# Optimization experiments

Measured on AMD Instinct MI355X. Metric: run time of the kernel, lower is better.

The kernel has to match this reference:

```python
import jax, jax.numpy as jnp
import numpy as np

MAX_NUM_ATOMS = 128  # static stand-in for tf's data-dependent max(pair_indices)+1


def setup_inputs() -> dict:
    key = jax.random.key(0)
    k1, k2 = jax.random.split(key)
    B, M, F = 32, 4096, 64
    edge_features = jax.random.normal(k1, (B, M, F), dtype=jnp.float32)
    pair_indices = jax.random.randint(k2, (B, M, 2), 0, MAX_NUM_ATOMS).astype(jnp.int64)
    return {"edge_features": edge_features, "pair_indices": pair_indices}


def reference(edge_features, pair_indices):
    # edge_features: [B, M, F]; pair_indices: [B, M, 2] with values in [0, N)
    B, M, F = edge_features.shape
    N = MAX_NUM_ATOMS
    b_idx = jnp.broadcast_to(jnp.arange(B)[:, None], (B, M))  # batch index per edge
    i_idx = pair_indices[..., 0]
    j_idx = pair_indices[..., 1]
    out = jnp.zeros((B, N, N, F), dtype=edge_features.dtype)
    # scatter-add each edge feature into dense [B, N, N, F] adjacency-feature tensor
    out = out.at[b_idx, i_idx, j_idx].add(edge_features)
    return out
```

## Files before the change

### kernel.cpp

```cpp
#include <hip/hip_runtime.h>

constexpr int B_DIM   = 32;
constexpr int M_EDGES = 4096;
constexpr int F_DIM   = 64;
constexpr int N_ATOMS = 128;

constexpr int TOTAL_EDGES = B_DIM * M_EDGES;
constexpr int CELLS       = B_DIM * N_ATOMS * N_ATOMS;
constexpr int K_CAP       = 16;

__global__ __launch_bounds__(256) void bin_edges_kernel(
    const int* __restrict__ pair,
    int*       __restrict__ counts,
    unsigned int* __restrict__ list)
{
    const int e = blockIdx.x * 256 + threadIdx.x;
    if (e >= TOTAL_EDGES) return;

    const int2 ij = ((const int2*)pair)[e];
    const int b = e >> 12;

    const int cell = (b << 14) + (ij.x << 7) + ij.y;

    const int pos = atomicAdd(&counts[cell], 1);
    if (pos < K_CAP) list[cell * K_CAP + pos] = (unsigned int)e;
}

__global__ __launch_bounds__(256) void gather_write_kernel(
    const float*        __restrict__ edge,
    const int*          __restrict__ counts,
    const unsigned int* __restrict__ list,
    float*              __restrict__ out)
{
    const int tid  = blockIdx.x * 256 + threadIdx.x;
    const int cell = tid >> 4;
    const int q    = tid & 15;

    int cnt = counts[cell];
    cnt = cnt > K_CAP ? K_CAP : cnt;

    float4 acc = make_float4(0.f, 0.f, 0.f, 0.f);
    const unsigned int* cl = list + (size_t)cell * K_CAP;

    for (int t = 0; t < cnt; ++t) {
        const unsigned int e = cl[t];
        const float4 v = ((const float4*)edge)[(size_t)e * 16 + q];
        acc.x += v.x; acc.y += v.y; acc.z += v.z; acc.w += v.w;
    }

    ((float4*)out)[(size_t)cell * 16 + q] = acc;
}

extern "C" void kernel_launch(void* const* d_in, const int* in_sizes, int n_in,
                              void* d_out, int out_size, void* d_ws, size_t ws_size,
                              hipStream_t stream) {
    const float* edge = (const float*)d_in[0];
    const int*   pair = (const int*)d_in[1];
    float*       out  = (float*)d_out;

    int*          counts = (int*)d_ws;
    unsigned int* list   = (unsigned int*)((char*)d_ws + (size_t)CELLS * sizeof(int));

    hipMemsetAsync(counts, 0, (size_t)CELLS * sizeof(int), stream);

    bin_edges_kernel<<<TOTAL_EDGES / 256, 256, 0, stream>>>(pair, counts, list);

    gather_write_kernel<<<(CELLS * 16) / 256, 256, 0, stream>>>(edge, counts, list, out);
}
```

Baseline: 46.14 us.

## Pack per-cell edge list into 8-byte record with global overflow pool

Replaces the per-cell count plus a 16-slot edge list with an 8-byte packed record per cell. The record holds a 16-bit count and up to three 16-bit in-batch edge indices, and any further edges go to a global overflow pool that is scanned linearly. The gather kernel reads one uint2 per cell and issues three branch-free loads, which shrinks workspace traffic and uses a single coalesced metadata read. The risk is the pool scan: any cell with more than three edges walks the whole pool. Edges beyond the pool capacity are silently dropped, and the atomicOr packing adds extra atomics.

```diff
diff --git a/kernel.cpp b/kernel.cpp
--- a/kernel.cpp
+++ b/kernel.cpp
@@ -7,48 +7,84 @@
 
 constexpr int TOTAL_EDGES = B_DIM * M_EDGES;
 constexpr int CELLS       = B_DIM * N_ATOMS * N_ATOMS;
-constexpr int K_CAP       = 16;
+constexpr unsigned int POOL_CAP = 8192;
+
+using f32x4 = __attribute__((ext_vector_type(4))) float;
+
 
 __global__ __launch_bounds__(256) void bin_edges_kernel(
-    const int* __restrict__ pair,
-    int*       __restrict__ counts,
-    unsigned int* __restrict__ list)
+    const int*          __restrict__ pair,
+    unsigned int*       __restrict__ packed,
+    unsigned int*       __restrict__ pool_cnt,
+    unsigned long long* __restrict__ pool)
 {
     const int e = blockIdx.x * 256 + threadIdx.x;
-    if (e >= TOTAL_EDGES) return;
-
     const int2 ij = ((const int2*)pair)[e];
     const int b = e >> 12;
+    const unsigned int m = (unsigned int)(e & (M_EDGES - 1));
 
-    const int cell = (b << 14) + (ij.x << 7) + ij.y;
+    const int cell = (b << 14) | (ij.x << 7) | ij.y;
+    unsigned int* rec = packed + 2 * (size_t)cell;
 
-    const int pos = atomicAdd(&counts[cell], 1);
-    if (pos < K_CAP) list[cell * K_CAP + pos] = (unsigned int)e;
+    const unsigned int old = atomicAdd(&rec[0], 1u);
+    const unsigned int pos = old & 0xFFFFu;
+
+    if (pos == 0u) {
+        atomicOr(&rec[0], m << 16);
+    } else if (pos == 1u) {
+        atomicOr(&rec[1], m);
+    } else if (pos == 2u) {
+        atomicOr(&rec[1], m << 16);
+    } else {
+        const unsigned int pi = atomicAdd(pool_cnt, 1u);
+        if (pi < POOL_CAP)
+            pool[pi] = ((unsigned long long)(unsigned int)cell << 32) | (unsigned int)e;
+    }
 }
 
 __global__ __launch_bounds__(256) void gather_write_kernel(
-    const float*        __restrict__ edge,
-    const int*          __restrict__ counts,
-    const unsigned int* __restrict__ list,
-    float*              __restrict__ out)
+    const float*              __restrict__ edge,
+    const unsigned int*       __restrict__ packed,
+    const unsigned int*       __restrict__ pool_cnt,
+    const unsigned long long* __restrict__ pool,
+    float*                    __restrict__ out)
 {
     const int tid  = blockIdx.x * 256 + threadIdx.x;
     const int cell = tid >> 4;
     const int q    = tid & 15;
 
-    int cnt = counts[cell];
-    cnt = cnt > K_CAP ? K_CAP : cnt;
+    const uint2 r = ((const uint2*)packed)[cell];
+    const int cnt = (int)(r.x & 0xFFFFu);
 
-    float4 acc = make_float4(0.f, 0.f, 0.f, 0.f);
-    const unsigned int* cl = list + (size_t)cell * K_CAP;
+    f32x4 acc = (f32x4)0.0f;
+    const f32x4* ef = (const f32x4*)edge;
 
-    for (int t = 0; t < cnt; ++t) {
-        const unsigned int e = cl[t];
-        const float4 v = ((const float4*)edge)[(size_t)e * 16 + q];
-        acc.x += v.x; acc.y += v.y; acc.z += v.z; acc.w += v.w;
+    if (cnt > 0) {
+        const int ebase = (cell >> 14) << 12;
+        const int e0 = ebase + (int)(r.x >> 16);
+        const int e1 = cnt > 1 ? ebase + (int)(r.y & 0xFFFFu) : e0;
+        const int e2 = cnt > 2 ? ebase + (int)(r.y >> 16)     : e0;
+
+        const f32x4 a0 = ef[(size_t)e0 * 16 + q];
+        const f32x4 a1 = ef[(size_t)e1 * 16 + q];
+        const f32x4 a2 = ef[(size_t)e2 * 16 + q];
+
+        acc = a0;
+        acc += a1 * (cnt > 1 ? 1.0f : 0.0f);
+        acc += a2 * (cnt > 2 ? 1.0f : 0.0f);
+
+        if (cnt > 3) {
+            unsigned int pc = *pool_cnt;
+            pc = pc > POOL_CAP ? POOL_CAP : pc;
+            for (unsigned int t = 0; t < pc; ++t) {
+                const unsigned long long ent = pool[t];
+                if ((int)(ent >> 32) == cell)
+                    acc += ef[(size_t)(unsigned int)ent * 16 + q];
+            }
+        }
     }
 
-    ((float4*)out)[(size_t)cell * 16 + q] = acc;
+    ((f32x4*)out)[(size_t)cell * 16 + q] = acc;
 }
 
 extern "C" void kernel_launch(void* const* d_in, const int* in_sizes, int n_in,
@@ -58,12 +94,13 @@
     const int*   pair = (const int*)d_in[1];
     float*       out  = (float*)d_out;
 
-    int*          counts = (int*)d_ws;
-    unsigned int* list   = (unsigned int*)((char*)d_ws + (size_t)CELLS * sizeof(int));
+    unsigned int*       packed   = (unsigned int*)d_ws;
+    unsigned int*       pool_cnt = (unsigned int*)((char*)d_ws + (size_t)CELLS * 8);
+    unsigned long long* pool     = (unsigned long long*)((char*)d_ws + (size_t)CELLS * 8 + 8);
 
-    hipMemsetAsync(counts, 0, (size_t)CELLS * sizeof(int), stream);
+    hipMemsetAsync(d_ws, 0, (size_t)CELLS * 8 + 16, stream);
 
-    bin_edges_kernel<<<TOTAL_EDGES / 256, 256, 0, stream>>>(pair, counts, list);
+    bin_edges_kernel<<<TOTAL_EDGES / 256, 256, 0, stream>>>(pair, packed, pool_cnt, pool);
 
-    gather_write_kernel<<<(CELLS * 16) / 256, 256, 0, stream>>>(edge, counts, list, out);
+    gather_write_kernel<<<(CELLS * 16) / 256, 256, 0, stream>>>(edge, packed, pool_cnt, pool, out);
 }
```

New measurement: 53.94 us. +16.9%, slower.

## Bin edges by half-row and accumulate dense tiles in shared memory

Applied to the files above, without the earlier changes.

Replaces per-cell binning (one counter and list slot per output cell) with half-row bins covering 64 j-columns, packing the local column and edge index into each list entry. The gather kernel assigns one block per bin, scatters edge features into a zeroed LDS tile with workgroup-scope atomics, then writes the 16 KB tile contiguously. This cuts the memset size, the count and list reads, and the per-cell overhead, at the cost of LDS atomics and a per-bin capacity limit of 64 edges.

```diff
diff --git a/kernel.cpp b/kernel.cpp
--- a/kernel.cpp
+++ b/kernel.cpp
@@ -6,49 +6,68 @@
 constexpr int N_ATOMS = 128;
 
 constexpr int TOTAL_EDGES = B_DIM * M_EDGES;
-constexpr int CELLS       = B_DIM * N_ATOMS * N_ATOMS;
-constexpr int K_CAP       = 16;
+constexpr int BINS  = B_DIM * N_ATOMS * 2;
+constexpr int K_CAP = 64;
+
+using f32x4 = __attribute__((ext_vector_type(4))) float;
 
 __global__ __launch_bounds__(256) void bin_edges_kernel(
-    const int* __restrict__ pair,
-    int*       __restrict__ counts,
+    const int*    __restrict__ pair,
+    int*          __restrict__ counts,
     unsigned int* __restrict__ list)
 {
     const int e = blockIdx.x * 256 + threadIdx.x;
-    if (e >= TOTAL_EDGES) return;
-
     const int2 ij = ((const int2*)pair)[e];
     const int b = e >> 12;
 
-    const int cell = (b << 14) + (ij.x << 7) + ij.y;
-
-    const int pos = atomicAdd(&counts[cell], 1);
-    if (pos < K_CAP) list[cell * K_CAP + pos] = (unsigned int)e;
+    const int bin = (b << 8) | (ij.x << 1) | (ij.y >> 6);
+    const int pos = atomicAdd(&counts[bin], 1);
+    if (pos < K_CAP)
+        list[bin * K_CAP + pos] =
+            (unsigned int)(((ij.y & 63) << 12) | (e & (M_EDGES - 1)));
 }
 
-__global__ __launch_bounds__(256) void gather_write_kernel(
+__global__ __launch_bounds__(256) void gather_halfrow_kernel(
     const float*        __restrict__ edge,
     const int*          __restrict__ counts,
     const unsigned int* __restrict__ list,
     float*              __restrict__ out)
 {
-    const int tid  = blockIdx.x * 256 + threadIdx.x;
-    const int cell = tid >> 4;
-    const int q    = tid & 15;
+    __shared__ float tile[64 * F_DIM];
+    __shared__ unsigned int q[K_CAP];
 
-    int cnt = counts[cell];
-    cnt = cnt > K_CAP ? K_CAP : cnt;
+    const int bin = (int)blockIdx.x;
+    const int tid = (int)threadIdx.x;
 
-    float4 acc = make_float4(0.f, 0.f, 0.f, 0.f);
-    const unsigned int* cl = list + (size_t)cell * K_CAP;
+    int cnt = counts[bin];
+    if (cnt > K_CAP) cnt = K_CAP;
 
-    for (int t = 0; t < cnt; ++t) {
-        const unsigned int e = cl[t];
-        const float4 v = ((const float4*)edge)[(size_t)e * 16 + q];
-        acc.x += v.x; acc.y += v.y; acc.z += v.z; acc.w += v.w;
+    if (tid < K_CAP) q[tid] = list[bin * K_CAP + tid];
+    f32x4* t4 = (f32x4*)tile;
+    #pragma unroll
+    for (int k = 0; k < 4; ++k)
+        t4[tid + 256 * k] = (f32x4)0.0f;
+    __syncthreads();
+
+    const int b    = bin >> 8;
+    const int lane = tid & 63;
+    const int wv   = tid >> 6;
+    const float* eb = edge + (size_t)b * M_EDGES * F_DIM;
+
+    for (int t = wv; t < cnt; t += 4) {
+        const unsigned int ent = q[t];
+        const int m  = (int)(ent & 4095u);
+        const int jl = (int)((ent >> 12) & 63u);
+        const float v = eb[m * F_DIM + lane];
+        __hip_atomic_fetch_add(&tile[(jl << 6) + lane], v,
+                               __ATOMIC_RELAXED, __HIP_MEMORY_SCOPE_WORKGROUP);
     }
+    __syncthreads();
 
-    ((float4*)out)[(size_t)cell * 16 + q] = acc;
+    f32x4* o4 = (f32x4*)(out + (size_t)bin * (64 * F_DIM));
+    #pragma unroll
+    for (int k = 0; k < 4; ++k)
+        o4[tid + 256 * k] = t4[tid + 256 * k];
 }
 
 extern "C" void kernel_launch(void* const* d_in, const int* in_sizes, int n_in,
@@ -59,11 +78,11 @@
     float*       out  = (float*)d_out;
 
     int*          counts = (int*)d_ws;
-    unsigned int* list   = (unsigned int*)((char*)d_ws + (size_t)CELLS * sizeof(int));
+    unsigned int* list   = (unsigned int*)((char*)d_ws + (size_t)BINS * sizeof(int));
 
-    hipMemsetAsync(counts, 0, (size_t)CELLS * sizeof(int), stream);
+    hipMemsetAsync(counts, 0, (size_t)BINS * sizeof(int), stream);
 
     bin_edges_kernel<<<TOTAL_EDGES / 256, 256, 0, stream>>>(pair, counts, list);
 
-    gather_write_kernel<<<(CELLS * 16) / 256, 256, 0, stream>>>(edge, counts, list, out);
+    gather_halfrow_kernel<<<BINS, 256, 0, stream>>>(edge, counts, list, out);
 }
```

Result: slower. 68.21 us (+47.8%).
